# Kernel optimization log

Hardware: AMD Instinct MI355X
Metric: run time of the kernel (lower is better)

## Reference

```python
import jax, jax.numpy as jnp
import numpy as np

HIDDEN = 1024
INTER = 1408
N_EXPERTS = 8
TOTAL_TOKENS = 8192


def setup_inputs() -> dict:
    key = jax.random.key(0)
    k_x, k_w1, k_w2 = jax.random.split(key, 3)
    x = jax.random.normal(k_x, (TOTAL_TOKENS, HIDDEN), dtype=jnp.float32)
    # fused gate+up projection per expert: [E, H, 2*I]
    w1w3 = jax.random.normal(k_w1, (N_EXPERTS, HIDDEN, 2 * INTER), dtype=jnp.float32) * (HIDDEN ** -0.5)
    # down projection per expert: [E, I, H]
    w2 = jax.random.normal(k_w2, (N_EXPERTS, INTER, HIDDEN), dtype=jnp.float32) * (INTER ** -0.5)
    # deterministic uneven split that sums exactly to TOTAL_TOKENS
    tpe = np.array([700, 1300, 900, 1100, 1024, 1024, 800, 1344], dtype=np.int64)
    assert tpe.sum() == TOTAL_TOKENS
    tokens_per_expert = jnp.asarray(tpe)
    return {"x": x, "w1w3": w1w3, "w2": w2, "tokens_per_expert": tokens_per_expert, "decoding": False}


def _grouped_mm(inp, W, expert_ids):
    # inp: [T, D_in], W: [E, D_in, D_out]; rows of inp are grouped by expert,
    # expert_ids[t] = owning expert. Equivalent to per-segment GEMM with W[e].
    T = inp.shape[0]
    E = W.shape[0]
    out = jnp.zeros((T, W.shape[-1]), dtype=inp.dtype)
    for e in range(E):  # fixed small expert count; loop over experts, not tokens
        mask = (expert_ids == e)[:, None]
        out = out + jnp.where(mask, inp, 0.0) @ W[e]
    return out


def reference(x, w1w3, w2, tokens_per_expert, decoding):
    T = x.shape[0]
    E = w1w3.shape[0]
    # per-token expert id from contiguous segment lengths (jit-safe fixed length)
    expert_ids = jnp.repeat(jnp.arange(E), tokens_per_expert, total_repeat_length=T)
    gate_up = _grouped_mm(x, w1w3, expert_ids)          # [T, 2*I]
    gate, up = jnp.split(gate_up, 2, axis=-1)           # swiglu(split_dim=-1)
    h = jax.nn.silu(gate) * up                          # [T, I]
    return _grouped_mm(h, w2, expert_ids)               # [T, H]
```

## Files before the change

### kernel.cpp

```cpp
#include <hip/hip_runtime.h>
#include <hip/hip_bf16.h>


#define HIDDEN 1024
#define INTER  1408
#define NEXP   8
#define TOKENS 8192

typedef __attribute__((ext_vector_type(8))) short bf16x8;
typedef __attribute__((ext_vector_type(4))) float f32x4;
typedef __attribute__((ext_vector_type(4))) unsigned short u16x4;
typedef __attribute__((ext_vector_type(8))) unsigned short u16x8;

#define GLOAD_LDS16(g, l)                                                      \
  __builtin_amdgcn_global_load_lds(                                            \
      (const __attribute__((address_space(1))) void*)(g),                      \
      (__attribute__((address_space(3))) void*)(l), 16, 0, 0)

__device__ inline unsigned short f2bf(float f) {
  unsigned int x = __float_as_uint(f);
  x += 0x7fffu + ((x >> 16) & 1u);
  return (unsigned short)(x >> 16);
}

__device__ inline int detect_f32(const float* __restrict__ xf, int lane) {
  unsigned int u = __float_as_uint(xf[lane & 63]);
  int e = (u >> 23) & 0xff;
  return __popcll(__ballot(e >= 100 && e <= 140)) >= 48 ? 1 : 0;
}

__device__ inline void load_tpe(const int* __restrict__ raw, int* tpe) {
  bool ok = true; int s = 0;
#pragma unroll
  for (int e = 0; e < NEXP; e++) { int v = raw[e]; tpe[e] = v; ok = ok && (v >= 0 && v <= TOKENS); s += v; }
  if (ok && s == TOKENS) return;
  ok = true; s = 0;
#pragma unroll
  for (int e = 0; e < NEXP; e++) { int v = raw[2 * e]; tpe[e] = v; ok = ok && (v >= 0 && v <= TOKENS); s += v; }
  if (ok && s == TOKENS) return;
  const int fb[NEXP] = {700, 1300, 900, 1100, 1024, 1024, 800, 1344};
#pragma unroll
  for (int e = 0; e < NEXP; e++) tpe[e] = fb[e];
}

__device__ inline bool expert_map(const int* __restrict__ tpe_raw, int rt,
                                  int& expert, int& row0, int& rows_valid) {
  int tpe[NEXP];
  load_tpe(tpe_raw, tpe);
  int acc = 0, pre = 0;
#pragma unroll
  for (int e = 0; e < NEXP; e++) {
    int nt = (tpe[e] + 127) >> 7;
    if (rt < acc + nt) {
      int ti = rt - acc;
      expert = e; row0 = pre + ti * 128; rows_valid = tpe[e] - ti * 128;
      return true;
    }
    acc += nt; pre += tpe[e];
  }
  return false;
}

__device__ inline void transpose_tile(const void* __restrict__ in,
                                      unsigned short* __restrict__ out,
                                      int R, int C, int r0, int c0,
                                      int t, int f32) {
  const int mr = t & 7, mc = t >> 3;
  const int r = r0 + mr * 8, c = c0 + mc * 4;
  u16x8 w[4];
  if (f32) {
    f32x4 fv[8];
#pragma unroll
    for (int i = 0; i < 8; i++)
      fv[i] = *(const f32x4*)((const float*)in + (size_t)(r + i) * C + c);
#pragma unroll
    for (int j = 0; j < 4; j++)
#pragma unroll
      for (int i = 0; i < 8; i++) w[j][i] = f2bf(fv[i][j]);
  } else {
    u16x4 uv[8];
#pragma unroll
    for (int i = 0; i < 8; i++)
      uv[i] = *(const u16x4*)((const unsigned short*)in + (size_t)(r + i) * C + c);
#pragma unroll
    for (int j = 0; j < 4; j++)
#pragma unroll
      for (int i = 0; i < 8; i++) w[j][i] = uv[i][j];
  }
#pragma unroll
  for (int j = 0; j < 4; j++)
    *(u16x8*)&out[(size_t)(c + j) * R + r] = w[j];
}

__global__ __launch_bounds__(256) void prepare(
    const float* __restrict__ xf, const void* __restrict__ x,
    const void* __restrict__ w1w3, const void* __restrict__ w2,
    unsigned short* __restrict__ xb, unsigned short* __restrict__ w1t,
    unsigned short* __restrict__ w2t) {
  const int t = threadIdx.x;
  const int f32 = detect_f32(xf, t & 63);
  const int b = blockIdx.x;

  if (b < 2048) {
    const size_t base = (size_t)b * 4096;
#pragma unroll
    for (int k = 0; k < 4; k++) {
      const size_t i = base + k * 1024 + t * 4;
      u16x4 v;
      if (f32) {
        f32x4 fv = *(const f32x4*)((const float*)x + i);
        v[0] = f2bf(fv[0]); v[1] = f2bf(fv[1]); v[2] = f2bf(fv[2]); v[3] = f2bf(fv[3]);
      } else {
        v = *(const u16x4*)((const unsigned short*)x + i);
      }
      *(u16x4*)(xb + i) = v;
    }
    return;
  }

  if (b < 4864) {
    const int u = b - 2048;
    const int ex = u / 352, rem = u % 352;
    const int r0 = (rem / 22) * 64, c0 = (rem % 22) * 128;
    const char* in = (const char*)w1w3 +
                     (size_t)ex * 1024 * 2816 * (f32 ? 4 : 2);
    transpose_tile(in, w1t + (size_t)ex * 2816 * 1024, 1024, 2816, r0, c0, t, f32);
  } else {
    const int u = b - 4864;
    const int ex = u / 176, rem = u % 176;
    const int r0 = (rem / 8) * 64, c0 = (rem % 8) * 128;
    const char* in = (const char*)w2 +
                     (size_t)ex * 1408 * 1024 * (f32 ? 4 : 2);
    transpose_tile(in, w2t + (size_t)ex * 1024 * 1408, 1408, 1024, r0, c0, t, f32);
  }
}

__global__ __launch_bounds__(256, 2) void moe_gemm1(
    const unsigned short* __restrict__ xb, const unsigned short* __restrict__ w1t,
    const int* __restrict__ tpe_raw, unsigned short* __restrict__ h) {
  __shared__ unsigned short As[128 * 32];
  __shared__ unsigned short Bg[64 * 32];
  __shared__ unsigned short Bu[64 * 32];
  int expert, row0, rows_valid;
  if (!expert_map(tpe_raw, blockIdx.y, expert, row0, rows_valid)) return;

  const int tid = threadIdx.x;
  const int lane = tid & 63, wave = tid >> 6;
  const int wr = wave >> 1, wc = wave & 1;
  const int i0 = blockIdx.x * 64;
  const unsigned short* W = w1t + (size_t)expert * 2816 * HIDDEN;

  const int q0 = wave * 2, q1 = wave * 2 + 1;
  const int sr0 = q0 * 16 + (lane >> 2), sr1 = q1 * 16 + (lane >> 2);
  const int sb = wave * 16 + (lane >> 2);
  const int sk = (lane & 3) * 8;
  const size_t arow0 = (size_t)min(row0 + sr0, TOKENS - 1);
  const size_t arow1 = (size_t)min(row0 + sr1, TOKENS - 1);
  const unsigned short* pa0 = xb + arow0 * HIDDEN + sk;
  const unsigned short* pa1 = xb + arow1 * HIDDEN + sk;
  const unsigned short* pg = W + (size_t)(i0 + sb) * HIDDEN + sk;
  const unsigned short* pu = W + (size_t)(INTER + i0 + sb) * HIDDEN + sk;

  f32x4 accg[4][2] = {};
  f32x4 accu[4][2] = {};
  const int fr = lane & 15, fq = (lane >> 4) * 8;

  for (int k0 = 0; k0 < HIDDEN; k0 += 32) {
    __syncthreads();
    GLOAD_LDS16(pa0, &As[q0 * 512]);
    GLOAD_LDS16(pa1, &As[q1 * 512]);
    GLOAD_LDS16(pg, &Bg[wave * 512]);
    GLOAD_LDS16(pu, &Bu[wave * 512]);
    pa0 += 32; pa1 += 32; pg += 32; pu += 32;
    __syncthreads();

    bf16x8 a[4], bg[2], bu[2];
#pragma unroll
    for (int mi = 0; mi < 4; mi++)
      a[mi] = *(const bf16x8*)&As[(wr * 64 + mi * 16 + fr) * 32 + fq];
#pragma unroll
    for (int ni = 0; ni < 2; ni++) {
      bg[ni] = *(const bf16x8*)&Bg[(wc * 32 + ni * 16 + fr) * 32 + fq];
      bu[ni] = *(const bf16x8*)&Bu[(wc * 32 + ni * 16 + fr) * 32 + fq];
    }
#pragma unroll
    for (int mi = 0; mi < 4; mi++)
#pragma unroll
      for (int ni = 0; ni < 2; ni++) {
        accg[mi][ni] =
            __builtin_amdgcn_mfma_f32_16x16x32_bf16(a[mi], bg[ni], accg[mi][ni], 0, 0, 0);
        accu[mi][ni] =
            __builtin_amdgcn_mfma_f32_16x16x32_bf16(a[mi], bu[ni], accu[mi][ni], 0, 0, 0);
      }
  }

#pragma unroll
  for (int mi = 0; mi < 4; mi++)
#pragma unroll
    for (int r = 0; r < 4; r++) {
      const int row_local = wr * 64 + mi * 16 + ((lane >> 4) * 4) + r;
      if (row_local < rows_valid && row0 + row_local < TOKENS) {
        const size_t rowoff = (size_t)(row0 + row_local) * INTER;
#pragma unroll
        for (int ni = 0; ni < 2; ni++) {
          const int col = i0 + wc * 32 + ni * 16 + fr;
          const float g = accg[mi][ni][r];
          const float u = accu[mi][ni][r];
          const float sg = g / (1.0f + __expf(-g));
          h[rowoff + col] = f2bf(sg * u);
        }
      }
    }
}

__global__ __launch_bounds__(256, 2) void moe_gemm2(
    const unsigned short* __restrict__ h, const unsigned short* __restrict__ w2t,
    const int* __restrict__ tpe_raw, void* __restrict__ out,
    const float* __restrict__ xf) {
  __shared__ unsigned short As[128 * 32];
  __shared__ unsigned short Bs[128 * 32];
  int expert, row0, rows_valid;
  if (!expert_map(tpe_raw, blockIdx.y, expert, row0, rows_valid)) return;
  const int f32out = detect_f32(xf, threadIdx.x & 63);

  const int tid = threadIdx.x;
  const int lane = tid & 63, wave = tid >> 6;
  const int wr = wave >> 1, wc = wave & 1;
  const int n0 = blockIdx.x * 128;
  const unsigned short* W = w2t + (size_t)expert * INTER * HIDDEN;

  const int q0 = wave * 2, q1 = wave * 2 + 1;
  const int sr0 = q0 * 16 + (lane >> 2), sr1 = q1 * 16 + (lane >> 2);
  const int sk = (lane & 3) * 8;
  const size_t arow0 = (size_t)min(row0 + sr0, TOKENS - 1);
  const size_t arow1 = (size_t)min(row0 + sr1, TOKENS - 1);
  const unsigned short* pa0 = h + arow0 * INTER + sk;
  const unsigned short* pa1 = h + arow1 * INTER + sk;
  const unsigned short* pb0 = W + (size_t)(n0 + sr0) * INTER + sk;
  const unsigned short* pb1 = W + (size_t)(n0 + sr1) * INTER + sk;

  f32x4 acc[4][4] = {};
  const int fr = lane & 15, fq = (lane >> 4) * 8;

  for (int k0 = 0; k0 < INTER; k0 += 32) {
    __syncthreads();
    GLOAD_LDS16(pa0, &As[q0 * 512]);
    GLOAD_LDS16(pa1, &As[q1 * 512]);
    GLOAD_LDS16(pb0, &Bs[q0 * 512]);
    GLOAD_LDS16(pb1, &Bs[q1 * 512]);
    pa0 += 32; pa1 += 32; pb0 += 32; pb1 += 32;
    __syncthreads();

    bf16x8 a[4], b[4];
#pragma unroll
    for (int mi = 0; mi < 4; mi++)
      a[mi] = *(const bf16x8*)&As[(wr * 64 + mi * 16 + fr) * 32 + fq];
#pragma unroll
    for (int ni = 0; ni < 4; ni++)
      b[ni] = *(const bf16x8*)&Bs[(wc * 64 + ni * 16 + fr) * 32 + fq];
#pragma unroll
    for (int mi = 0; mi < 4; mi++)
#pragma unroll
      for (int ni = 0; ni < 4; ni++)
        acc[mi][ni] =
            __builtin_amdgcn_mfma_f32_16x16x32_bf16(a[mi], b[ni], acc[mi][ni], 0, 0, 0);
  }

#pragma unroll
  for (int mi = 0; mi < 4; mi++)
#pragma unroll
    for (int r = 0; r < 4; r++) {
      const int row_local = wr * 64 + mi * 16 + ((lane >> 4) * 4) + r;
      if (row_local < rows_valid && row0 + row_local < TOKENS) {
        const size_t rowoff = (size_t)(row0 + row_local) * HIDDEN;
#pragma unroll
        for (int ni = 0; ni < 4; ni++) {
          const int col = n0 + wc * 64 + ni * 16 + fr;
          if (f32out)
            ((float*)out)[rowoff + col] = acc[mi][ni][r];
          else
            ((unsigned short*)out)[rowoff + col] = f2bf(acc[mi][ni][r]);
        }
      }
    }
}

extern "C" void kernel_launch(void* const* d_in, const int* in_sizes, int n_in,
                              void* d_out, int out_size, void* d_ws, size_t ws_size,
                              hipStream_t stream) {
  const void* x = d_in[0];
  const void* w1w3 = d_in[1];
  const void* w2 = d_in[2];
  const int* tpe = (const int*)d_in[3];
  const float* xf = (const float*)d_in[0];

  const size_t XB_BYTES = (size_t)TOKENS * HIDDEN * 2;
  const size_t W1T_BYTES = (size_t)NEXP * 2816 * HIDDEN * 2;
  const size_t W2T_BYTES = (size_t)NEXP * INTER * HIDDEN * 2;
  char* ws = (char*)d_ws;
  unsigned short* xb = (unsigned short*)ws;
  unsigned short* w1t = (unsigned short*)(ws + XB_BYTES);
  unsigned short* w2t = (unsigned short*)(ws + XB_BYTES + W1T_BYTES);
  unsigned short* h = (unsigned short*)(ws + XB_BYTES + W1T_BYTES + W2T_BYTES);

  prepare<<<6272, 256, 0, stream>>>(xf, x, w1w3, w2, xb, w1t, w2t);
  moe_gemm1<<<dim3(INTER / 64, 72), 256, 0, stream>>>(xb, w1t, tpe, h);
  moe_gemm2<<<dim3(HIDDEN / 128, 72), 256, 0, stream>>>(h, w2t, tpe, d_out, xf);
}
```

Measured before the change: 327.5 us.

## Double-buffer LDS tiles in both GEMMs and widen prepare-kernel vector accesses

Both grouped GEMM kernels now use two LDS buffers and issue the global-to-LDS loads for the next K tile before computing on the current one, with one barrier per iteration instead of two. This aims to hide global load latency behind MFMA work, at the cost of doubling shared memory per block, which may lower occupancy. Separately, the prepare kernel now handles 8 columns per thread in both the conversion and transpose paths, with 16-byte vector loads and stores. This halves its grid size and gives fewer, wider memory transactions.

Result: no change. 331.8 us (+1.3%).

```diff
diff --git a/kernel.cpp b/kernel.cpp
--- a/kernel.cpp
+++ b/kernel.cpp
@@ -66,29 +66,35 @@
                                       int R, int C, int r0, int c0,
                                       int t, int f32) {
   const int mr = t & 7, mc = t >> 3;
-  const int r = r0 + mr * 8, c = c0 + mc * 4;
-  u16x8 w[4];
+  const int r = r0 + mr * 8, c = c0 + mc * 8;
+  u16x8 w[8];
   if (f32) {
-    f32x4 fv[8];
+    f32x4 f0[8], f1[8];
+#pragma unroll
+    for (int i = 0; i < 8; i++) {
+      const float* p = (const float*)in + (size_t)(r + i) * C + c;
+      f0[i] = *(const f32x4*)p;
+      f1[i] = *(const f32x4*)(p + 4);
+    }
+#pragma unroll
+    for (int j = 0; j < 4; j++)
+#pragma unroll
+      for (int i = 0; i < 8; i++) {
+        w[j][i]     = f2bf(f0[i][j]);
+        w[j + 4][i] = f2bf(f1[i][j]);
+      }
+  } else {
+    u16x8 uv[8];
 #pragma unroll
     for (int i = 0; i < 8; i++)
-      fv[i] = *(const f32x4*)((const float*)in + (size_t)(r + i) * C + c);
-#pragma unroll
-    for (int j = 0; j < 4; j++)
-#pragma unroll
-      for (int i = 0; i < 8; i++) w[j][i] = f2bf(fv[i][j]);
-  } else {
-    u16x4 uv[8];
-#pragma unroll
-    for (int i = 0; i < 8; i++)
-      uv[i] = *(const u16x4*)((const unsigned short*)in + (size_t)(r + i) * C + c);
-#pragma unroll
-    for (int j = 0; j < 4; j++)
+      uv[i] = *(const u16x8*)((const unsigned short*)in + (size_t)(r + i) * C + c);
+#pragma unroll
+    for (int j = 0; j < 8; j++)
 #pragma unroll
       for (int i = 0; i < 8; i++) w[j][i] = uv[i][j];
   }
 #pragma unroll
-  for (int j = 0; j < 4; j++)
+  for (int j = 0; j < 8; j++)
     *(u16x8*)&out[(size_t)(c + j) * R + r] = w[j];
 }
 
@@ -101,34 +107,36 @@
   const int f32 = detect_f32(xf, t & 63);
   const int b = blockIdx.x;
 
-  if (b < 2048) {
-    const size_t base = (size_t)b * 4096;
+  if (b < 1024) {
+    const size_t base = (size_t)b * 8192;
 #pragma unroll
     for (int k = 0; k < 4; k++) {
-      const size_t i = base + k * 1024 + t * 4;
-      u16x4 v;
+      const size_t i = base + k * 2048 + t * 8;
+      u16x8 v;
       if (f32) {
-        f32x4 fv = *(const f32x4*)((const float*)x + i);
-        v[0] = f2bf(fv[0]); v[1] = f2bf(fv[1]); v[2] = f2bf(fv[2]); v[3] = f2bf(fv[3]);
+        f32x4 g0 = *(const f32x4*)((const float*)x + i);
+        f32x4 g1 = *(const f32x4*)((const float*)x + i + 4);
+#pragma unroll
+        for (int j = 0; j < 4; j++) { v[j] = f2bf(g0[j]); v[j + 4] = f2bf(g1[j]); }
       } else {
-        v = *(const u16x4*)((const unsigned short*)x + i);
-      }
-      *(u16x4*)(xb + i) = v;
+        v = *(const u16x8*)((const unsigned short*)x + i);
+      }
+      *(u16x8*)(xb + i) = v;
     }
     return;
   }
 
-  if (b < 4864) {
-    const int u = b - 2048;
-    const int ex = u / 352, rem = u % 352;
-    const int r0 = (rem / 22) * 64, c0 = (rem % 22) * 128;
+  if (b < 2432) {
+    const int u = b - 1024;
+    const int ex = u / 176, rem = u % 176;
+    const int r0 = (rem / 11) * 64, c0 = (rem % 11) * 256;
     const char* in = (const char*)w1w3 +
                      (size_t)ex * 1024 * 2816 * (f32 ? 4 : 2);
     transpose_tile(in, w1t + (size_t)ex * 2816 * 1024, 1024, 2816, r0, c0, t, f32);
   } else {
-    const int u = b - 4864;
-    const int ex = u / 176, rem = u % 176;
-    const int r0 = (rem / 8) * 64, c0 = (rem % 8) * 128;
+    const int u = b - 2432;
+    const int ex = u / 88, rem = u % 88;
+    const int r0 = (rem / 4) * 64, c0 = (rem % 4) * 256;
     const char* in = (const char*)w2 +
                      (size_t)ex * 1408 * 1024 * (f32 ? 4 : 2);
     transpose_tile(in, w2t + (size_t)ex * 1024 * 1408, 1408, 1024, r0, c0, t, f32);
@@ -138,9 +146,9 @@
 __global__ __launch_bounds__(256, 2) void moe_gemm1(
     const unsigned short* __restrict__ xb, const unsigned short* __restrict__ w1t,
     const int* __restrict__ tpe_raw, unsigned short* __restrict__ h) {
-  __shared__ unsigned short As[128 * 32];
-  __shared__ unsigned short Bg[64 * 32];
-  __shared__ unsigned short Bu[64 * 32];
+  __shared__ unsigned short As[2][128 * 32];
+  __shared__ unsigned short Bg[2][64 * 32];
+  __shared__ unsigned short Bu[2][64 * 32];
   int expert, row0, rows_valid;
   if (!expert_map(tpe_raw, blockIdx.y, expert, row0, rows_valid)) return;
 
@@ -165,23 +173,32 @@
   f32x4 accu[4][2] = {};
   const int fr = lane & 15, fq = (lane >> 4) * 8;
 
-  for (int k0 = 0; k0 < HIDDEN; k0 += 32) {
-    __syncthreads();
-    GLOAD_LDS16(pa0, &As[q0 * 512]);
-    GLOAD_LDS16(pa1, &As[q1 * 512]);
-    GLOAD_LDS16(pg, &Bg[wave * 512]);
-    GLOAD_LDS16(pu, &Bu[wave * 512]);
-    pa0 += 32; pa1 += 32; pg += 32; pu += 32;
-    __syncthreads();
+  GLOAD_LDS16(pa0, &As[0][q0 * 512]);
+  GLOAD_LDS16(pa1, &As[0][q1 * 512]);
+  GLOAD_LDS16(pg, &Bg[0][wave * 512]);
+  GLOAD_LDS16(pu, &Bu[0][wave * 512]);
+  pa0 += 32; pa1 += 32; pg += 32; pu += 32;
+  __syncthreads();
+
+  const int NT = HIDDEN / 32;
+  for (int it = 0; it < NT; ++it) {
+    const int cur = it & 1, nxt = cur ^ 1;
+    if (it + 1 < NT) {
+      GLOAD_LDS16(pa0, &As[nxt][q0 * 512]);
+      GLOAD_LDS16(pa1, &As[nxt][q1 * 512]);
+      GLOAD_LDS16(pg, &Bg[nxt][wave * 512]);
+      GLOAD_LDS16(pu, &Bu[nxt][wave * 512]);
+      pa0 += 32; pa1 += 32; pg += 32; pu += 32;
+    }
 
     bf16x8 a[4], bg[2], bu[2];
 #pragma unroll
     for (int mi = 0; mi < 4; mi++)
-      a[mi] = *(const bf16x8*)&As[(wr * 64 + mi * 16 + fr) * 32 + fq];
+      a[mi] = *(const bf16x8*)&As[cur][(wr * 64 + mi * 16 + fr) * 32 + fq];
 #pragma unroll
     for (int ni = 0; ni < 2; ni++) {
-      bg[ni] = *(const bf16x8*)&Bg[(wc * 32 + ni * 16 + fr) * 32 + fq];
-      bu[ni] = *(const bf16x8*)&Bu[(wc * 32 + ni * 16 + fr) * 32 + fq];
+      bg[ni] = *(const bf16x8*)&Bg[cur][(wc * 32 + ni * 16 + fr) * 32 + fq];
+      bu[ni] = *(const bf16x8*)&Bu[cur][(wc * 32 + ni * 16 + fr) * 32 + fq];
     }
 #pragma unroll
     for (int mi = 0; mi < 4; mi++)
@@ -192,6 +209,8 @@
         accu[mi][ni] =
             __builtin_amdgcn_mfma_f32_16x16x32_bf16(a[mi], bu[ni], accu[mi][ni], 0, 0, 0);
       }
+
+    __syncthreads();
   }
 
 #pragma unroll
@@ -217,8 +236,8 @@
     const unsigned short* __restrict__ h, const unsigned short* __restrict__ w2t,
     const int* __restrict__ tpe_raw, void* __restrict__ out,
     const float* __restrict__ xf) {
-  __shared__ unsigned short As[128 * 32];
-  __shared__ unsigned short Bs[128 * 32];
+  __shared__ unsigned short As[2][128 * 32];
+  __shared__ unsigned short Bs[2][128 * 32];
   int expert, row0, rows_valid;
   if (!expert_map(tpe_raw, blockIdx.y, expert, row0, rows_valid)) return;
   const int f32out = detect_f32(xf, threadIdx.x & 63);
@@ -242,28 +261,39 @@
   f32x4 acc[4][4] = {};
   const int fr = lane & 15, fq = (lane >> 4) * 8;
 
-  for (int k0 = 0; k0 < INTER; k0 += 32) {
-    __syncthreads();
-    GLOAD_LDS16(pa0, &As[q0 * 512]);
-    GLOAD_LDS16(pa1, &As[q1 * 512]);
-    GLOAD_LDS16(pb0, &Bs[q0 * 512]);
-    GLOAD_LDS16(pb1, &Bs[q1 * 512]);
-    pa0 += 32; pa1 += 32; pb0 += 32; pb1 += 32;
-    __syncthreads();
-
-    bf16x8 a[4], b[4];
+  GLOAD_LDS16(pa0, &As[0][q0 * 512]);
+  GLOAD_LDS16(pa1, &As[0][q1 * 512]);
+  GLOAD_LDS16(pb0, &Bs[0][q0 * 512]);
+  GLOAD_LDS16(pb1, &Bs[0][q1 * 512]);
+  pa0 += 32; pa1 += 32; pb0 += 32; pb1 += 32;
+  __syncthreads();
+
+  const int NT = INTER / 32;
+  for (int it = 0; it < NT; ++it) {
+    const int cur = it & 1, nxt = cur ^ 1;
+    if (it + 1 < NT) {
+      GLOAD_LDS16(pa0, &As[nxt][q0 * 512]);
+      GLOAD_LDS16(pa1, &As[nxt][q1 * 512]);
+      GLOAD_LDS16(pb0, &Bs[nxt][q0 * 512]);
+      GLOAD_LDS16(pb1, &Bs[nxt][q1 * 512]);
+      pa0 += 32; pa1 += 32; pb0 += 32; pb1 += 32;
+    }
+
+    bf16x8 a[4], bb[4];
 #pragma unroll
     for (int mi = 0; mi < 4; mi++)
-      a[mi] = *(const bf16x8*)&As[(wr * 64 + mi * 16 + fr) * 32 + fq];
+      a[mi] = *(const bf16x8*)&As[cur][(wr * 64 + mi * 16 + fr) * 32 + fq];
 #pragma unroll
     for (int ni = 0; ni < 4; ni++)
-      b[ni] = *(const bf16x8*)&Bs[(wc * 64 + ni * 16 + fr) * 32 + fq];
+      bb[ni] = *(const bf16x8*)&Bs[cur][(wc * 64 + ni * 16 + fr) * 32 + fq];
 #pragma unroll
     for (int mi = 0; mi < 4; mi++)
 #pragma unroll
       for (int ni = 0; ni < 4; ni++)
         acc[mi][ni] =
-            __builtin_amdgcn_mfma_f32_16x16x32_bf16(a[mi], b[ni], acc[mi][ni], 0, 0, 0);
+            __builtin_amdgcn_mfma_f32_16x16x32_bf16(a[mi], bb[ni], acc[mi][ni], 0, 0, 0);
+
+    __syncthreads();
   }
 
 #pragma unroll
@@ -303,7 +333,7 @@
   unsigned short* w2t = (unsigned short*)(ws + XB_BYTES + W1T_BYTES);
   unsigned short* h = (unsigned short*)(ws + XB_BYTES + W1T_BYTES + W2T_BYTES);
 
-  prepare<<<6272, 256, 0, stream>>>(xf, x, w1w3, w2, xb, w1t, w2t);
+  prepare<<<3136, 256, 0, stream>>>(xf, x, w1w3, w2, xb, w1t, w2t);
   moe_gemm1<<<dim3(INTER / 64, 72), 256, 0, stream>>>(xb, w1t, tpe, h);
   moe_gemm2<<<dim3(HIDDEN / 128, 72), 256, 0, stream>>>(h, w2t, tpe, d_out, xf);
 }
```
